# Kernel tuning notes

Hardware: AMD Instinct MI355X
Metric: run time of the kernel (lower is better)

The kernel has to match this reference:

```python
import jax, jax.numpy as jnp
import numpy as np

NL, DM, DI, DS, DR, DC = 4, 1024, 2048, 16, 64, 4
B, L, DLOC, NC = 8, 224, 672, 10
EPS = 1e-5


def _rmsnorm(h, w):
    return h * jax.lax.rsqrt(jnp.mean(h * h, axis=-1, keepdims=True) + EPS) * w


def setup_inputs() -> dict:
    key = jax.random.key(0)
    ks = jax.random.split(key, 10)
    s = 0.02
    return dict(
        x=jax.random.normal(ks[0], (B, L, DLOC), jnp.float32),
        w_proj=jax.random.normal(ks[1], (DLOC, DM), jnp.float32) * s,
        b_proj=jnp.zeros((DM,), jnp.float32),
        norm_w=jnp.ones((NL, DM), jnp.float32),
        w_in=jax.random.normal(ks[2], (NL, DM, 2 * DI), jnp.float32) * s,
        w_conv=jax.random.normal(ks[3], (NL, DI, DC), jnp.float32) * s,
        b_conv=jnp.zeros((NL, DI), jnp.float32),
        w_x=jax.random.normal(ks[4], (NL, DI, DR + 2 * DS), jnp.float32) * s,
        w_dt=jax.random.normal(ks[5], (NL, DR, DI), jnp.float32) * s,
        b_dt=jax.random.normal(ks[6], (NL, DI), jnp.float32) * 0.1,
        A_log=jnp.broadcast_to(jnp.log(jnp.arange(1, DS + 1, dtype=jnp.float32)), (NL, DI, DS)) + jnp.zeros((NL, DI, DS), jnp.float32),
        Dp=jnp.ones((NL, DI), jnp.float32),
        w_out=jax.random.normal(ks[7], (NL, DI, DM), jnp.float32) * s,
        final_norm_w=jnp.ones((DM,), jnp.float32),
        w_fc=jax.random.normal(ks[8], (DM, NC), jnp.float32) * s,
        b_fc=jnp.zeros((NC,), jnp.float32),
    )


def reference(x, w_proj, b_proj, norm_w, w_in, w_conv, b_conv, w_x, w_dt, b_dt, A_log, Dp, w_out, final_norm_w, w_fc, b_fc):
    # input_proj: (B,L,DLOC) -> (B,L,DM)
    h = x @ w_proj + b_proj
    for l in range(NL):
        xn = _rmsnorm(h, norm_w[l])
        xz = xn @ w_in[l]                      # (B,L,2*DI)
        xp, z = jnp.split(xz, 2, axis=-1)
        # causal depthwise conv1d along L, kernel size DC
        xpad = jnp.pad(xp, ((0, 0), (DC - 1, 0), (0, 0)))
        xc = sum(xpad[:, k:k + L, :] * w_conv[l][:, k] for k in range(DC)) + b_conv[l]
        xc = jax.nn.silu(xc)
        x_dbl = xc @ w_x[l]                    # (B,L,DR+2*DS)
        dtr, Bm, Cm = jnp.split(x_dbl, [DR, DR + DS], axis=-1)
        dt = jax.nn.softplus(dtr @ w_dt[l] + b_dt[l])   # (B,L,DI)
        A = -jnp.exp(A_log[l])                 # (DI,DS)
        xs = (jnp.swapaxes(dt, 0, 1), jnp.swapaxes(Bm, 0, 1),
              jnp.swapaxes(Cm, 0, 1), jnp.swapaxes(xc, 0, 1))

        def step(hs, inp):
            dt_t, B_t, C_t, u_t = inp          # (B,DI),(B,DS),(B,DS),(B,DI)
            dA = jnp.exp(dt_t[:, :, None] * A)                        # (B,DI,DS)
            hs = dA * hs + (dt_t * u_t)[:, :, None] * B_t[:, None, :]
            y = jnp.einsum('bds,bs->bd', hs, C_t)
            return hs, y

        h0 = jnp.zeros((B, DI, DS), x.dtype)
        _, ys = jax.lax.scan(step, h0, xs)     # ys: (L,B,DI)
        y = jnp.swapaxes(ys, 0, 1) + Dp[l] * xc
        y = y * jax.nn.silu(z)
        h = h + y @ w_out[l]
    h = _rmsnorm(h, final_norm_w)
    pooled = h[:, -1, :]                       # last-token pooling
    return pooled @ w_fc + b_fc                # (B,NC)
```

## Files before the change

### kernel.cpp

```cpp
#include <hip/hip_runtime.h>
#include <hip/hip_bf16.h>
#include <hip/hip_fp16.h>
#include <math.h>

#define NL 4
#define DM 1024
#define DI 2048
#define DS 16
#define DR 64
#define DC 4
#define B_ 8
#define L_ 224
#define DLOC 672
#define NC 10
#define EPS 1e-5f

#define ROWS (B_ * L_)

typedef unsigned short u16;
typedef __attribute__((ext_vector_type(8))) short bf16x8;
typedef __attribute__((ext_vector_type(4))) float f32x4;
typedef __attribute__((address_space(1))) const void gvoid_t;
typedef __attribute__((address_space(3))) void lvoid_t;

__device__ __forceinline__ u16 f2bf(float f) {
  union { float f; unsigned int u; } v;
  v.f = f;
  unsigned int u = v.u;
  return (u16)((u + 0x7fffu + ((u >> 16) & 1u)) >> 16);
}

__device__ __forceinline__ void load4h(const __half* p, float* o) {
  uint2 r = *(const uint2*)p;
  __half2 h0 = *(__half2*)&r.x;
  __half2 h1 = *(__half2*)&r.y;
  float2 f0 = __half22float2(h0);
  float2 f1 = __half22float2(h1);
  o[0] = f0.x; o[1] = f0.y; o[2] = f1.x; o[3] = f1.y;
}

__device__ __forceinline__ void load8h(const __half* p, float* o) {
  uint4 r = *(const uint4*)p;
  __half2 h0 = *(__half2*)&r.x;
  __half2 h1 = *(__half2*)&r.y;
  __half2 h2 = *(__half2*)&r.z;
  __half2 h3 = *(__half2*)&r.w;
  float2 f0 = __half22float2(h0);
  float2 f1 = __half22float2(h1);
  float2 f2 = __half22float2(h2);
  float2 f3 = __half22float2(h3);
  o[0] = f0.x; o[1] = f0.y; o[2] = f1.x; o[3] = f1.y;
  o[4] = f2.x; o[5] = f2.y; o[6] = f3.x; o[7] = f3.y;
}

template <int ACC, int BROW, int TSTORE, int ACT, int SPLITK, typename OT>
__global__ __launch_bounds__(256) void gemm_bt_mfma(
    const u16* __restrict__ A, const u16* __restrict__ Bt,
    const float* __restrict__ bias, OT* __restrict__ C, int K, int lda,
    int ldb, int ldc) {
  if (SPLITK) {
    A += (size_t)blockIdx.z * SPLITK;
    Bt += (size_t)blockIdx.z * SPLITK;
  }
  __shared__ __align__(16) u16 As[128 * 32];
  __shared__ __align__(16) u16 Bs[128 * 32];
  const int tid = threadIdx.x;
  const int lane = tid & 63;
  const int wv = tid >> 6;
  const int n0 = blockIdx.x * 128;
  const int m0 = blockIdx.y * 128;
  const int wm0 = (wv & 1) * 64;
  const int wn0 = (wv >> 1) * 64;
  const int quad = lane >> 4;
  const int l16 = lane & 15;

  const int srow = wv * 32 + (lane >> 2);
  const int scol = (lane & 3) * 8;
  const u16* ga0 = A + (size_t)(m0 + srow) * lda + scol;
  const u16* ga1 = ga0 + (size_t)16 * lda;
  const u16* gb0 = Bt + (size_t)(n0 + srow) * ldb + scol;
  const u16* gb1 = gb0 + (size_t)16 * ldb;
  u16* la0 = &As[(wv * 32) * 32];
  u16* la1 = &As[(wv * 32 + 16) * 32];
  u16* lb0 = &Bs[(wv * 32) * 32];
  u16* lb1 = &Bs[(wv * 32 + 16) * 32];

  f32x4 acc[4][4] = {};

  for (int k0 = 0; k0 < K; k0 += 32) {
    __syncthreads();
    __builtin_amdgcn_global_load_lds((gvoid_t*)ga0, (lvoid_t*)la0, 16, 0, 0);
    __builtin_amdgcn_global_load_lds((gvoid_t*)ga1, (lvoid_t*)la1, 16, 0, 0);
    __builtin_amdgcn_global_load_lds((gvoid_t*)gb0, (lvoid_t*)lb0, 16, 0, 0);
    __builtin_amdgcn_global_load_lds((gvoid_t*)gb1, (lvoid_t*)lb1, 16, 0, 0);
    __syncthreads();
    bf16x8 af[4], bfr[4];
#pragma unroll
    for (int i = 0; i < 4; i++)
      af[i] = *(const bf16x8*)&As[(wm0 + i * 16 + l16) * 32 + quad * 8];
#pragma unroll
    for (int j = 0; j < 4; j++)
      bfr[j] = *(const bf16x8*)&Bs[(wn0 + j * 16 + l16) * 32 + quad * 8];
#pragma unroll
    for (int i = 0; i < 4; i++)
#pragma unroll
      for (int j = 0; j < 4; j++)
        acc[i][j] = __builtin_amdgcn_mfma_f32_16x16x32_bf16(af[i], bfr[j],
                                                            acc[i][j], 0, 0, 0);
    ga0 += 32; ga1 += 32; gb0 += 32; gb1 += 32;
  }

#pragma unroll
  for (int i = 0; i < 4; i++) {
#pragma unroll
    for (int j = 0; j < 4; j++) {
      const int col = n0 + wn0 + j * 16 + l16;
      const int rowb = m0 + wm0 + i * 16 + quad * 4;
      if (TSTORE) {
        __half* Ch = (__half*)C;
        union { __half2 h[2]; uint2 u; } pk;
        pk.h[0].x = __float2half(acc[i][j][0]);
        pk.h[0].y = __float2half(acc[i][j][1]);
        pk.h[1].x = __float2half(acc[i][j][2]);
        pk.h[1].y = __float2half(acc[i][j][3]);
        *(uint2*)(Ch + (size_t)col * ldc + rowb) = pk.u;
      } else {
        float bv = 0.f;
        if (BROW == 1) bv = bias[col];
#pragma unroll
        for (int r = 0; r < 4; r++) {
          float v = acc[i][j][r] + bv;
          if (BROW == 2) v += bias[rowb + r];
          if (ACT == 1) v = (v > 20.f) ? v : log1pf(expf(v));
          OT* p = C + (size_t)(rowb + r) * ldc + col;
          if (ACC == 2) {
            atomicAdd((float*)p, v);
          } else {
            if (ACC == 1) v += (float)*p;
            *p = (OT)v;
          }
        }
      }
    }
  }
}

__device__ __forceinline__ void transpose_cvt_body(
    const float* __restrict__ src, u16* __restrict__ dst, int K, int N,
    int bx, int by, int tid) {
  __shared__ float t[32][33];
  const int n0 = bx * 32;
  const int k0 = by * 32;
  const int c = tid & 31;
  const int r = tid >> 5;
#pragma unroll
  for (int rr = 0; rr < 4; rr++)
    t[r + rr * 8][c] = src[(size_t)(k0 + r + rr * 8) * N + n0 + c];
  __syncthreads();
#pragma unroll
  for (int rr = 0; rr < 4; rr++)
    dst[(size_t)(n0 + r + rr * 8) * K + k0 + c] = f2bf(t[c][r + rr * 8]);
}

__global__ __launch_bounds__(256) void transpose_cvt_kernel(
    const float* __restrict__ src, u16* __restrict__ dst, int K, int N) {
  transpose_cvt_body(src, dst, K, N, blockIdx.x, blockIdx.y, threadIdx.x);
}

__global__ __launch_bounds__(256) void prep_weights_kernel(
    const float* __restrict__ w_in_l, const float* __restrict__ w_out_l,
    const float* __restrict__ w_x_l, const float* __restrict__ w_dt_l,
    u16* __restrict__ winT, u16* __restrict__ woutT, u16* __restrict__ w_x16,
    u16* __restrict__ w_dt16) {
  int bid = blockIdx.x;
  if (bid < 4096) {
    transpose_cvt_body(w_in_l, winT, DM, 2 * DI, bid & 127, bid >> 7,
                       threadIdx.x);
  } else if (bid < 6144) {
    bid -= 4096;
    transpose_cvt_body(w_out_l, woutT, DI, DM, bid & 31, bid >> 5,
                       threadIdx.x);
  } else if (bid < 6336) {
    bid -= 6144;
    transpose_cvt_body(w_x_l, w_x16, DI, 96, bid % 3, bid / 3, threadIdx.x);
  } else {
    bid -= 6336;
    transpose_cvt_body(w_dt_l, w_dt16, DR, DI, bid & 63, bid >> 6,
                       threadIdx.x);
  }
}

__global__ __launch_bounds__(256) void transpose_u16_kernel(
    const u16* __restrict__ src, u16* __restrict__ dst, int K, int N) {
  __shared__ u16 t[32][33];
  const int n0 = blockIdx.x * 32;
  const int k0 = blockIdx.y * 32;
  const int c = threadIdx.x & 31;
  const int r = threadIdx.x >> 5;
#pragma unroll
  for (int rr = 0; rr < 4; rr++)
    t[r + rr * 8][c] = src[(size_t)(k0 + r + rr * 8) * N + n0 + c];
  __syncthreads();
#pragma unroll
  for (int rr = 0; rr < 4; rr++)
    dst[(size_t)(n0 + r + rr * 8) * K + k0 + c] = t[c][r + rr * 8];
}

__global__ __launch_bounds__(256) void cvt_kernel(const float* __restrict__ src,
                                                  u16* __restrict__ dst) {
  const int i = blockIdx.x * 256 + threadIdx.x;
  const float4 v = ((const float4*)src)[i];
  ushort4 o;
  o.x = f2bf(v.x);
  o.y = f2bf(v.y);
  o.z = f2bf(v.z);
  o.w = f2bf(v.w);
  ((ushort4*)dst)[i] = o;
}

__global__ __launch_bounds__(256) void rmsnorm_kernel(
    const float* __restrict__ h, const float* __restrict__ w,
    u16* __restrict__ out) {
  const int row = blockIdx.x;
  const int tid = threadIdx.x;
  const float4 v = *(const float4*)(h + (size_t)row * DM + tid * 4);
  float ss = v.x * v.x + v.y * v.y + v.z * v.z + v.w * v.w;
#pragma unroll
  for (int off = 32; off > 0; off >>= 1) ss += __shfl_xor(ss, off);
  __shared__ float red[4];
  if ((tid & 63) == 0) red[tid >> 6] = ss;
  __syncthreads();
  float tot = red[0] + red[1] + red[2] + red[3];
  const float inv = rsqrtf(tot / (float)DM + EPS);
  const float4 wv = *(const float4*)(w + tid * 4);
  ushort4 o;
  o.x = f2bf(v.x * inv * wv.x);
  o.y = f2bf(v.y * inv * wv.y);
  o.z = f2bf(v.z * inv * wv.z);
  o.w = f2bf(v.w * inv * wv.w);
  *(ushort4*)(out + (size_t)row * DM + tid * 4) = o;
}

__global__ __launch_bounds__(256) void conv_silu_tile_kernel(
    const __half* __restrict__ xpT, const float* __restrict__ wc,
    const float* __restrict__ bc, __half* __restrict__ uT,
    u16* __restrict__ u16rm) {
  __shared__ u16 tile[32][33];
  const int tid = threadIdx.x;
  const int d0 = blockIdx.x * 32;
  const int r0 = blockIdx.y * 32;
  const int dl = tid >> 3;
  const int rq = (tid & 7) * 4;
  const int d = d0 + dl;
  const int r = r0 + rq;
  const int t = r % L_;
  const __half* row = xpT + (size_t)d * ROWS + r;
  float v[4];
  load4h(row, v);
  float p0 = 0.f, p1 = 0.f, p2 = 0.f;
  if (t > 0) {
    p0 = __half2float(row[-3]);
    p1 = __half2float(row[-2]);
    p2 = __half2float(row[-1]);
  }
  const float w0 = wc[d * 4 + 0], w1 = wc[d * 4 + 1], w2 = wc[d * 4 + 2],
              w3 = wc[d * 4 + 3];
  const float bb = bc[d];
  float o[4];
  float s;
  s = bb + p0 * w0 + p1 * w1 + p2 * w2 + v[0] * w3; o[0] = s / (1.f + expf(-s));
  s = bb + p1 * w0 + p2 * w1 + v[0] * w2 + v[1] * w3; o[1] = s / (1.f + expf(-s));
  s = bb + p2 * w0 + v[0] * w1 + v[1] * w2 + v[2] * w3; o[2] = s / (1.f + expf(-s));
  s = bb + v[0] * w0 + v[1] * w1 + v[2] * w2 + v[3] * w3; o[3] = s / (1.f + expf(-s));
  union { __half2 h[2]; uint2 u; } pk;
  pk.h[0].x = __float2half(o[0]); pk.h[0].y = __float2half(o[1]);
  pk.h[1].x = __float2half(o[2]); pk.h[1].y = __float2half(o[3]);
  *(uint2*)(uT + (size_t)d * ROWS + r) = pk.u;
#pragma unroll
  for (int i = 0; i < 4; i++) tile[rq + i][dl] = f2bf(o[i]);
  __syncthreads();
  const int rl = tid >> 3;
  const int dq = (tid & 7) * 4;
  ushort4 ov;
  ov.x = tile[rl][dq + 0];
  ov.y = tile[rl][dq + 1];
  ov.z = tile[rl][dq + 2];
  ov.w = tile[rl][dq + 3];
  *(ushort4*)(u16rm + (size_t)(r0 + rl) * DI + d0 + dq) = ov;
}

__global__ __launch_bounds__(256) void scan_kernel(
    const __half* __restrict__ dtT, const __half* __restrict__ uT,
    const __half* __restrict__ zT, const float* __restrict__ xdblT,
    const float* __restrict__ A_log, const float* __restrict__ Dp,
    u16* __restrict__ yT) {
  __shared__ __align__(16) __half dtu[4][2][512];
  __shared__ __align__(16) __half zbuf[4][2][512];
  __shared__ __align__(16) float bcb[2][32 * 36];

  const int tid = threadIdx.x;
  const int wv = tid >> 6;
  const int lane = tid & 63;
  const int b = blockIdx.x >> 6;
  const int d0 = ((blockIdx.x & 63) << 5) + wv * 8;
  const int c = lane >> 3;
  const int sg = lane & 7;
  const int d = d0 + c;
  const int s0 = sg * 2;

  const int sl = lane & 31;
  const size_t srcoff =
      (size_t)(d0 + (sl & 7)) * ROWS + (size_t)b * L_ + (sl >> 3) * 8;
  const __half* gdtu = (lane < 32 ? dtT : uT) + srcoff;
  const __half* gz = zT + srcoff;

  const int bs = tid >> 3;
  const int bt4 = (tid & 7) * 4;
  const float* gbc = xdblT + (size_t)(DR + bs) * ROWS + (size_t)b * L_ + bt4;

  const float2 Al = *(const float2*)(A_log + (size_t)d * DS + s0);
  const float A20 = -expf(Al.x) * 1.44269504f;
  const float A21 = -expf(Al.y) * 1.44269504f;
  const float Dpd = Dp[d];
  u16* yp = yT + (size_t)d * ROWS + b * L_;

  float hs0 = 0.f, hs1 = 0.f;

  auto stage_dtuz = [&](int t0, int p) {
    __builtin_amdgcn_global_load_lds((gvoid_t*)(gdtu + t0),
                                     (lvoid_t*)&dtu[wv][p][0], 16, 0, 0);
    __builtin_amdgcn_global_load_lds((gvoid_t*)(gz + t0),
                                     (lvoid_t*)&zbuf[wv][p][0], 16, 0, 0);
  };

  {
    float4 bc0 = *(const float4*)gbc;
    stage_dtuz(0, 0);
    __builtin_amdgcn_s_waitcnt(0x0f70);
    *(float4*)&bcb[0][bs * 36 + bt4] = bc0;
    __syncthreads();
  }

  for (int ch = 0; ch < L_ / 32; ch++) {
    const int p = ch & 1;
    const int t0 = ch * 32;
    float4 bcn;
    const bool more = (ch + 1 < L_ / 32);
    if (more) {
      bcn = *(const float4*)(gbc + t0 + 32);
      stage_dtuz(t0 + 32, p ^ 1);
    }
#pragma unroll
    for (int g = 0; g < 4; g++) {
      float dt8[8], u8[8], z8[8];
      load8h(&dtu[wv][p][g * 64 + c * 8], dt8);
      load8h(&dtu[wv][p][256 + g * 64 + c * 8], u8);
      load8h(&zbuf[wv][p][g * 64 + c * 8], z8);
      float Bv0[8], Bv1[8], Cv0[8], Cv1[8];
      *(float4*)&Bv0[0] = *(const float4*)&bcb[p][s0 * 36 + g * 8];
      *(float4*)&Bv0[4] = *(const float4*)&bcb[p][s0 * 36 + g * 8 + 4];
      *(float4*)&Bv1[0] = *(const float4*)&bcb[p][(s0 + 1) * 36 + g * 8];
      *(float4*)&Bv1[4] = *(const float4*)&bcb[p][(s0 + 1) * 36 + g * 8 + 4];
      *(float4*)&Cv0[0] = *(const float4*)&bcb[p][(16 + s0) * 36 + g * 8];
      *(float4*)&Cv0[4] = *(const float4*)&bcb[p][(16 + s0) * 36 + g * 8 + 4];
      *(float4*)&Cv1[0] = *(const float4*)&bcb[p][(17 + s0) * 36 + g * 8];
      *(float4*)&Cv1[4] = *(const float4*)&bcb[p][(17 + s0) * 36 + g * 8 + 4];
      union { u16 h[8]; uint4 v; } yb;
#pragma unroll
      for (int k = 0; k < 8; k++) {
        const float dtv = dt8[k];
        const float uu = u8[k];
        const float du = dtv * uu;
        hs0 = fmaf(hs0, exp2f(dtv * A20), du * Bv0[k]);
        hs1 = fmaf(hs1, exp2f(dtv * A21), du * Bv1[k]);
        float pr = fmaf(hs1, Cv1[k], hs0 * Cv0[k]);
        pr += __shfl_xor(pr, 1);
        pr += __shfl_xor(pr, 2);
        pr += __shfl_xor(pr, 4);
        if (sg == 0) {
          const float zz = z8[k];
          float yv = pr + Dpd * uu;
          yv *= zz / (1.f + expf(-zz));
          yb.h[k] = f2bf(yv);
        }
      }
      if (sg == 0) *(uint4*)(yp + t0 + g * 8) = yb.v;
    }
    if (more) {
      __builtin_amdgcn_s_waitcnt(0x0f70);
      *(float4*)&bcb[p ^ 1][bs * 36 + bt4] = bcn;
    }
    __syncthreads();
  }
}

__global__ __launch_bounds__(256) void final_kernel(
    const float* __restrict__ h, const float* __restrict__ fnw,
    const float* __restrict__ w_fc, const float* __restrict__ b_fc,
    float* __restrict__ out) {
  const int b = blockIdx.x;
  const int tid = threadIdx.x;
  const size_t row = ((size_t)b * L_ + (L_ - 1)) * DM;
  const float4 v = *(const float4*)(h + row + tid * 4);
  float ss = v.x * v.x + v.y * v.y + v.z * v.z + v.w * v.w;
#pragma unroll
  for (int off = 32; off > 0; off >>= 1) ss += __shfl_xor(ss, off);
  __shared__ float red[4];
  if ((tid & 63) == 0) red[tid >> 6] = ss;
  __syncthreads();
  float tot = red[0] + red[1] + red[2] + red[3];
  const float inv = rsqrtf(tot / (float)DM + EPS);
  const float4 wv = *(const float4*)(fnw + tid * 4);
  float hn[4] = {v.x * inv * wv.x, v.y * inv * wv.y, v.z * inv * wv.z,
                 v.w * inv * wv.w};
  float partial[NC];
#pragma unroll
  for (int j = 0; j < NC; j++) partial[j] = 0.f;
#pragma unroll
  for (int e = 0; e < 4; e++) {
    const int dd = tid * 4 + e;
#pragma unroll
    for (int j = 0; j < NC; j++)
      partial[j] = fmaf(hn[e], w_fc[dd * NC + j], partial[j]);
  }
  __shared__ float red2[256][NC];
  for (int j = 0; j < NC; j++) red2[tid][j] = partial[j];
  __syncthreads();
  for (int stride = 128; stride > 0; stride >>= 1) {
    if (tid < stride)
      for (int j = 0; j < NC; j++) red2[tid][j] += red2[tid + stride][j];
    __syncthreads();
  }
  if (tid < NC) out[b * NC + tid] = red2[0][tid] + b_fc[tid];
}

extern "C" void kernel_launch(void* const* d_in, const int* in_sizes, int n_in,
                              void* d_out, int out_size, void* d_ws,
                              size_t ws_size, hipStream_t stream) {
  const float* x = (const float*)d_in[0];
  const float* w_proj = (const float*)d_in[1];
  const float* b_proj = (const float*)d_in[2];
  const float* norm_w = (const float*)d_in[3];
  const float* w_in = (const float*)d_in[4];
  const float* w_conv = (const float*)d_in[5];
  const float* b_conv = (const float*)d_in[6];
  const float* w_x = (const float*)d_in[7];
  const float* w_dt = (const float*)d_in[8];
  const float* b_dt = (const float*)d_in[9];
  const float* A_log = (const float*)d_in[10];
  const float* Dp = (const float*)d_in[11];
  const float* w_out = (const float*)d_in[12];
  const float* fnw = (const float*)d_in[13];
  const float* w_fc = (const float*)d_in[14];
  const float* b_fc = (const float*)d_in[15];
  float* out = (float*)d_out;

  float* ws = (float*)d_ws;
  float* h = ws;
  float* p1 = h + 1835008;
  __half* xzT = (__half*)p1;
  float* p2 = p1 + 3670016;
  __half* uT = (__half*)p2;
  float* p3 = p2 + 1835008;
  float* xdblT = p3;
  float* p4 = p3 + 229376;
  __half* dtT = (__half*)p4;
  float* p5 = p4 + 1835008;
  u16* yT = (u16*)p5;
  float* p6 = p5 + 1835008;
  u16* y16 = (u16*)p6;
  u16* xn16 = y16;
  float* p7 = p6 + 1835008;
  u16* u16rm = (u16*)p7;
  float* p8 = p7 + 1835008;
  u16* x16 = (u16*)p8;
  float* p9 = p8 + 602112;
  u16* wprojT = (u16*)p9;
  float* p10 = p9 + 344064;
  u16* winT = (u16*)p10;
  float* p11 = p10 + 2097152;
  u16* woutT = (u16*)p11;
  float* p12 = p11 + 1048576;
  u16* w_x16 = (u16*)p12;
  float* p13 = p12 + 131072;
  u16* w_dt16 = (u16*)p13;
  float* p14 = p13 + 65536;
  u16* dtr16 = (u16*)p14;

  const dim3 blk(256);

  cvt_kernel<<<ROWS * DLOC / 1024, blk, 0, stream>>>(x, x16);
  transpose_cvt_kernel<<<dim3(DM / 32, DLOC / 32), blk, 0, stream>>>(
      w_proj, wprojT, DLOC, DM);

  gemm_bt_mfma<0, 1, 0, 0, 0, float>
      <<<dim3(DM / 128, ROWS / 128), blk, 0, stream>>>(
          x16, wprojT, b_proj, h, DLOC, DLOC, DLOC, DM);

  for (int l = 0; l < NL; l++) {
    prep_weights_kernel<<<6464, blk, 0, stream>>>(
        w_in + (size_t)l * DM * 2 * DI, w_out + (size_t)l * DI * DM,
        w_x + (size_t)l * DI * 96, w_dt + (size_t)l * DR * DI, winT, woutT,
        w_x16, w_dt16);

    rmsnorm_kernel<<<ROWS, blk, 0, stream>>>(h, norm_w + (size_t)l * DM, xn16);
    gemm_bt_mfma<0, 0, 1, 0, 0, __half>
        <<<dim3(2 * DI / 128, ROWS / 128), blk, 0, stream>>>(
            xn16, winT, nullptr, (__half*)xzT, DM, DM, DM, ROWS);
    conv_silu_tile_kernel<<<dim3(DI / 32, ROWS / 32), blk, 0, stream>>>(
        xzT, w_conv + (size_t)l * DI * DC, b_conv + (size_t)l * DI, uT, u16rm);
    hipMemsetAsync(xdblT, 0, (size_t)128 * ROWS * sizeof(float), stream);
    gemm_bt_mfma<2, 0, 0, 0, 512, float>
        <<<dim3(ROWS / 128, 1, 4), blk, 0, stream>>>(
            w_x16, u16rm, nullptr, xdblT, 512, DI, DI, ROWS);
    transpose_cvt_kernel<<<dim3(ROWS / 32, DR / 32), blk, 0, stream>>>(
        xdblT, dtr16, DR, ROWS);
    gemm_bt_mfma<0, 2, 0, 1, 0, __half>
        <<<dim3(ROWS / 128, DI / 128), blk, 0, stream>>>(
            w_dt16, dtr16, b_dt + (size_t)l * DI, dtT, DR, DR, DR, ROWS);
    scan_kernel<<<dim3(B_ * (DI / 32)), blk, 0, stream>>>(
        dtT, uT, xzT + (size_t)DI * ROWS, xdblT, A_log + (size_t)l * DI * DS,
        Dp + (size_t)l * DI, yT);
    transpose_u16_kernel<<<dim3(ROWS / 32, DI / 32), blk, 0, stream>>>(
        yT, y16, DI, ROWS);
    gemm_bt_mfma<1, 0, 0, 0, 0, float>
        <<<dim3(DM / 128, ROWS / 128), blk, 0, stream>>>(
            y16, woutT, nullptr, h, DI, DI, DI, DM);
  }

  final_kernel<<<B_, blk, 0, stream>>>(h, fnw, w_fc, b_fc, out);
}
```

Measured before the change: 1.069 ms.

## Replace sequential selective scan with chunked three-pass scan in row-major layout

Replaces the single sequential scan kernel with a chunked parallel scan. A per-chunk state pass computes 16-step partial states and summed dt, a combine pass propagates carries across 14 chunks, and an apply pass recomputes outputs from the carried-in states. Intermediates (z, u, dt, y) move to row-major layout, which removes the y transpose kernel and the transposed dtr conversion, and the in-projection GEMM is split into separate x and z outputs. The goal is far more parallelism across the L dimension and fewer transpose passes, at the cost of extra state traffic and recomputing the recurrence twice.

```diff
diff --git a/kernel.cpp b/kernel.cpp
--- a/kernel.cpp
+++ b/kernel.cpp
@@ -16,6 +16,8 @@
 #define EPS 1e-5f
 
 #define ROWS (B_ * L_)
+#define NCHK 14
+#define CHS 16
 
 typedef unsigned short u16;
 typedef __attribute__((ext_vector_type(8))) short bf16x8;
@@ -37,20 +39,6 @@
   float2 f0 = __half22float2(h0);
   float2 f1 = __half22float2(h1);
   o[0] = f0.x; o[1] = f0.y; o[2] = f1.x; o[3] = f1.y;
-}
-
-__device__ __forceinline__ void load8h(const __half* p, float* o) {
-  uint4 r = *(const uint4*)p;
-  __half2 h0 = *(__half2*)&r.x;
-  __half2 h1 = *(__half2*)&r.y;
-  __half2 h2 = *(__half2*)&r.z;
-  __half2 h3 = *(__half2*)&r.w;
-  float2 f0 = __half22float2(h0);
-  float2 f1 = __half22float2(h1);
-  float2 f2 = __half22float2(h2);
-  float2 f3 = __half22float2(h3);
-  o[0] = f0.x; o[1] = f0.y; o[2] = f1.x; o[3] = f1.y;
-  o[4] = f2.x; o[5] = f2.y; o[6] = f3.x; o[7] = f3.y;
 }
 
 template <int ACC, int BROW, int TSTORE, int ACT, int SPLITK, typename OT>
@@ -190,22 +178,6 @@
   }
 }
 
-__global__ __launch_bounds__(256) void transpose_u16_kernel(
-    const u16* __restrict__ src, u16* __restrict__ dst, int K, int N) {
-  __shared__ u16 t[32][33];
-  const int n0 = blockIdx.x * 32;
-  const int k0 = blockIdx.y * 32;
-  const int c = threadIdx.x & 31;
-  const int r = threadIdx.x >> 5;
-#pragma unroll
-  for (int rr = 0; rr < 4; rr++)
-    t[r + rr * 8][c] = src[(size_t)(k0 + r + rr * 8) * N + n0 + c];
-  __syncthreads();
-#pragma unroll
-  for (int rr = 0; rr < 4; rr++)
-    dst[(size_t)(n0 + r + rr * 8) * K + k0 + c] = t[c][r + rr * 8];
-}
-
 __global__ __launch_bounds__(256) void cvt_kernel(const float* __restrict__ src,
                                                   u16* __restrict__ dst) {
   const int i = blockIdx.x * 256 + threadIdx.x;
@@ -218,6 +190,16 @@
   ((ushort4*)dst)[i] = o;
 }
 
+__global__ __launch_bounds__(256) void cvt_dtr_kernel(
+    const float* __restrict__ x_dbl, u16* __restrict__ dtr) {
+  const int e = (blockIdx.x * 256 + threadIdx.x) * 4;
+  const int r = e >> 6, cc = e & 63;
+  const float4 v = *(const float4*)(x_dbl + (size_t)r * 128 + cc);
+  ushort4 o;
+  o.x = f2bf(v.x); o.y = f2bf(v.y); o.z = f2bf(v.z); o.w = f2bf(v.w);
+  *(ushort4*)(dtr + (size_t)r * 64 + cc) = o;
+}
+
 __global__ __launch_bounds__(256) void rmsnorm_kernel(
     const float* __restrict__ h, const float* __restrict__ w,
     u16* __restrict__ out) {
@@ -243,9 +225,10 @@
 
 __global__ __launch_bounds__(256) void conv_silu_tile_kernel(
     const __half* __restrict__ xpT, const float* __restrict__ wc,
-    const float* __restrict__ bc, __half* __restrict__ uT,
-    u16* __restrict__ u16rm) {
+    const float* __restrict__ bc, u16* __restrict__ u16rm,
+    __half* __restrict__ u_rm) {
   __shared__ u16 tile[32][33];
+  __shared__ u16 tileh[32][33];
   const int tid = threadIdx.x;
   const int d0 = blockIdx.x * 32;
   const int r0 = blockIdx.y * 32;
@@ -272,125 +255,174 @@
   s = bb + p1 * w0 + p2 * w1 + v[0] * w2 + v[1] * w3; o[1] = s / (1.f + expf(-s));
   s = bb + p2 * w0 + v[0] * w1 + v[1] * w2 + v[2] * w3; o[2] = s / (1.f + expf(-s));
   s = bb + v[0] * w0 + v[1] * w1 + v[2] * w2 + v[3] * w3; o[3] = s / (1.f + expf(-s));
-  union { __half2 h[2]; uint2 u; } pk;
-  pk.h[0].x = __float2half(o[0]); pk.h[0].y = __float2half(o[1]);
-  pk.h[1].x = __float2half(o[2]); pk.h[1].y = __float2half(o[3]);
-  *(uint2*)(uT + (size_t)d * ROWS + r) = pk.u;
-#pragma unroll
-  for (int i = 0; i < 4; i++) tile[rq + i][dl] = f2bf(o[i]);
+#pragma unroll
+  for (int i = 0; i < 4; i++) {
+    tile[rq + i][dl] = f2bf(o[i]);
+    tileh[rq + i][dl] = __half_as_ushort(__float2half(o[i]));
+  }
   __syncthreads();
   const int rl = tid >> 3;
   const int dq = (tid & 7) * 4;
-  ushort4 ov;
+  ushort4 ov, oh;
   ov.x = tile[rl][dq + 0];
   ov.y = tile[rl][dq + 1];
   ov.z = tile[rl][dq + 2];
   ov.w = tile[rl][dq + 3];
+  oh.x = tileh[rl][dq + 0];
+  oh.y = tileh[rl][dq + 1];
+  oh.z = tileh[rl][dq + 2];
+  oh.w = tileh[rl][dq + 3];
   *(ushort4*)(u16rm + (size_t)(r0 + rl) * DI + d0 + dq) = ov;
-}
-
-__global__ __launch_bounds__(256) void scan_kernel(
-    const __half* __restrict__ dtT, const __half* __restrict__ uT,
-    const __half* __restrict__ zT, const float* __restrict__ xdblT,
+  *(ushort4*)((u16*)u_rm + (size_t)(r0 + rl) * DI + d0 + dq) = oh;
+}
+
+__global__ __launch_bounds__(64) void scan_state_kernel(
+    const __half* __restrict__ dt_rm, const __half* __restrict__ u_rm,
+    const float* __restrict__ x_dbl, const float* __restrict__ A_log,
+    float* __restrict__ S, float* __restrict__ sumdt) {
+  __shared__ u16 dts[CHS][64];
+  __shared__ u16 us[CHS][64];
+  __shared__ float Bs[CHS][16];
+  const int lane = threadIdx.x;
+  const int c = blockIdx.x, g = blockIdx.y, b = blockIdx.z;
+  const int d = (g << 6) + lane;
+  const size_t rbase = (size_t)b * L_ + c * CHS;
+  {
+    const int tr = lane >> 3, c8 = (lane & 7) << 3;
+    const size_t ro = (rbase + tr) * DI + (g << 6) + c8;
+    *(uint4*)&dts[tr][c8] = *(const uint4*)(dt_rm + ro);
+    *(uint4*)&dts[tr + 8][c8] = *(const uint4*)(dt_rm + ro + (size_t)8 * DI);
+    *(uint4*)&us[tr][c8] = *(const uint4*)(u_rm + ro);
+    *(uint4*)&us[tr + 8][c8] = *(const uint4*)(u_rm + ro + (size_t)8 * DI);
+    const int tb = lane >> 2, q4 = (lane & 3) << 2;
+    *(float4*)&Bs[tb][q4] =
+        *(const float4*)(x_dbl + (rbase + tb) * 128 + 64 + q4);
+  }
+  float A2[DS];
+  const float* al = A_log + (size_t)d * DS;
+#pragma unroll
+  for (int s = 0; s < DS; s++) A2[s] = -expf(al[s]) * 1.44269504f;
+  __syncthreads();
+
+  float hs[DS];
+#pragma unroll
+  for (int s = 0; s < DS; s++) hs[s] = 0.f;
+  float cd = 0.f;
+#pragma unroll 4
+  for (int t = 0; t < CHS; t++) {
+    const float dtv = __half2float(((const __half*)dts)[t * 64 + lane]);
+    const float uu = __half2float(((const __half*)us)[t * 64 + lane]);
+    const float du = dtv * uu;
+    cd += dtv;
+    const float4 B0 = *(const float4*)&Bs[t][0];
+    const float4 B1 = *(const float4*)&Bs[t][4];
+    const float4 B2 = *(const float4*)&Bs[t][8];
+    const float4 B3 = *(const float4*)&Bs[t][12];
+    auto upd = [&](int s0, float4 Bq) {
+      hs[s0 + 0] = fmaf(hs[s0 + 0], exp2f(dtv * A2[s0 + 0]), du * Bq.x);
+      hs[s0 + 1] = fmaf(hs[s0 + 1], exp2f(dtv * A2[s0 + 1]), du * Bq.y);
+      hs[s0 + 2] = fmaf(hs[s0 + 2], exp2f(dtv * A2[s0 + 2]), du * Bq.z);
+      hs[s0 + 3] = fmaf(hs[s0 + 3], exp2f(dtv * A2[s0 + 3]), du * Bq.w);
+    };
+    upd(0, B0); upd(4, B1); upd(8, B2); upd(12, B3);
+  }
+  float* Sp = S + (((size_t)c * B_ + b) * DI + d) * DS;
+#pragma unroll
+  for (int s = 0; s < DS; s++) Sp[s] = hs[s];
+  sumdt[((size_t)c * B_ + b) * DI + d] = cd;
+}
+
+__global__ __launch_bounds__(256) void scan_combine_kernel(
+    float* __restrict__ S, const float* __restrict__ sumdt,
+    const float* __restrict__ A_log) {
+  const int idx = blockIdx.x * 256 + threadIdx.x;
+  const int s = idx & 15;
+  const int d = (idx >> 4) & (DI - 1);
+  const int b = idx >> 15;
+  const float A2 = -expf(A_log[(size_t)d * DS + s]) * 1.44269504f;
+  float hv = 0.f;
+#pragma unroll
+  for (int c = 0; c < NCHK; c++) {
+    const size_t base = ((size_t)c * B_ + b) * DI + d;
+    const size_t ix = base * DS + s;
+    const float Sc = S[ix];
+    const float Dc = exp2f(A2 * sumdt[base]);
+    S[ix] = hv;
+    hv = fmaf(Dc, hv, Sc);
+  }
+}
+
+__global__ __launch_bounds__(64) void scan_apply_kernel(
+    const __half* __restrict__ dt_rm, const __half* __restrict__ u_rm,
+    const __half* __restrict__ z_rm, const float* __restrict__ x_dbl,
     const float* __restrict__ A_log, const float* __restrict__ Dp,
-    u16* __restrict__ yT) {
-  __shared__ __align__(16) __half dtu[4][2][512];
-  __shared__ __align__(16) __half zbuf[4][2][512];
-  __shared__ __align__(16) float bcb[2][32 * 36];
-
-  const int tid = threadIdx.x;
-  const int wv = tid >> 6;
-  const int lane = tid & 63;
-  const int b = blockIdx.x >> 6;
-  const int d0 = ((blockIdx.x & 63) << 5) + wv * 8;
-  const int c = lane >> 3;
-  const int sg = lane & 7;
-  const int d = d0 + c;
-  const int s0 = sg * 2;
-
-  const int sl = lane & 31;
-  const size_t srcoff =
-      (size_t)(d0 + (sl & 7)) * ROWS + (size_t)b * L_ + (sl >> 3) * 8;
-  const __half* gdtu = (lane < 32 ? dtT : uT) + srcoff;
-  const __half* gz = zT + srcoff;
-
-  const int bs = tid >> 3;
-  const int bt4 = (tid & 7) * 4;
-  const float* gbc = xdblT + (size_t)(DR + bs) * ROWS + (size_t)b * L_ + bt4;
-
-  const float2 Al = *(const float2*)(A_log + (size_t)d * DS + s0);
-  const float A20 = -expf(Al.x) * 1.44269504f;
-  const float A21 = -expf(Al.y) * 1.44269504f;
+    const float* __restrict__ HS, u16* __restrict__ y_rm) {
+  __shared__ u16 dts[CHS][64];
+  __shared__ u16 us[CHS][64];
+  __shared__ u16 zs[CHS][64];
+  __shared__ float Bs[CHS][16];
+  __shared__ float Cs[CHS][16];
+  const int lane = threadIdx.x;
+  const int c = blockIdx.x, g = blockIdx.y, b = blockIdx.z;
+  const int d = (g << 6) + lane;
+  const size_t rbase = (size_t)b * L_ + c * CHS;
+  {
+    const int tr = lane >> 3, c8 = (lane & 7) << 3;
+    const size_t ro = (rbase + tr) * DI + (g << 6) + c8;
+    *(uint4*)&dts[tr][c8] = *(const uint4*)(dt_rm + ro);
+    *(uint4*)&dts[tr + 8][c8] = *(const uint4*)(dt_rm + ro + (size_t)8 * DI);
+    *(uint4*)&us[tr][c8] = *(const uint4*)(u_rm + ro);
+    *(uint4*)&us[tr + 8][c8] = *(const uint4*)(u_rm + ro + (size_t)8 * DI);
+    *(uint4*)&zs[tr][c8] = *(const uint4*)(z_rm + ro);
+    *(uint4*)&zs[tr + 8][c8] = *(const uint4*)(z_rm + ro + (size_t)8 * DI);
+    const int tb = lane >> 2, q4 = (lane & 3) << 2;
+    *(float4*)&Bs[tb][q4] =
+        *(const float4*)(x_dbl + (rbase + tb) * 128 + 64 + q4);
+    *(float4*)&Cs[tb][q4] =
+        *(const float4*)(x_dbl + (rbase + tb) * 128 + 80 + q4);
+  }
+  float A2[DS];
+  const float* al = A_log + (size_t)d * DS;
+#pragma unroll
+  for (int s = 0; s < DS; s++) A2[s] = -expf(al[s]) * 1.44269504f;
+  float hs[DS];
+  const float* hp = HS + (((size_t)c * B_ + b) * DI + d) * DS;
+#pragma unroll
+  for (int s = 0; s < DS; s++) hs[s] = hp[s];
   const float Dpd = Dp[d];
-  u16* yp = yT + (size_t)d * ROWS + b * L_;
-
-  float hs0 = 0.f, hs1 = 0.f;
-
-  auto stage_dtuz = [&](int t0, int p) {
-    __builtin_amdgcn_global_load_lds((gvoid_t*)(gdtu + t0),
-                                     (lvoid_t*)&dtu[wv][p][0], 16, 0, 0);
-    __builtin_amdgcn_global_load_lds((gvoid_t*)(gz + t0),
-                                     (lvoid_t*)&zbuf[wv][p][0], 16, 0, 0);
-  };
-
-  {
-    float4 bc0 = *(const float4*)gbc;
-    stage_dtuz(0, 0);
-    __builtin_amdgcn_s_waitcnt(0x0f70);
-    *(float4*)&bcb[0][bs * 36 + bt4] = bc0;
-    __syncthreads();
-  }
-
-  for (int ch = 0; ch < L_ / 32; ch++) {
-    const int p = ch & 1;
-    const int t0 = ch * 32;
-    float4 bcn;
-    const bool more = (ch + 1 < L_ / 32);
-    if (more) {
-      bcn = *(const float4*)(gbc + t0 + 32);
-      stage_dtuz(t0 + 32, p ^ 1);
-    }
-#pragma unroll
-    for (int g = 0; g < 4; g++) {
-      float dt8[8], u8[8], z8[8];
-      load8h(&dtu[wv][p][g * 64 + c * 8], dt8);
-      load8h(&dtu[wv][p][256 + g * 64 + c * 8], u8);
-      load8h(&zbuf[wv][p][g * 64 + c * 8], z8);
-      float Bv0[8], Bv1[8], Cv0[8], Cv1[8];
-      *(float4*)&Bv0[0] = *(const float4*)&bcb[p][s0 * 36 + g * 8];
-      *(float4*)&Bv0[4] = *(const float4*)&bcb[p][s0 * 36 + g * 8 + 4];
-      *(float4*)&Bv1[0] = *(const float4*)&bcb[p][(s0 + 1) * 36 + g * 8];
-      *(float4*)&Bv1[4] = *(const float4*)&bcb[p][(s0 + 1) * 36 + g * 8 + 4];
-      *(float4*)&Cv0[0] = *(const float4*)&bcb[p][(16 + s0) * 36 + g * 8];
-      *(float4*)&Cv0[4] = *(const float4*)&bcb[p][(16 + s0) * 36 + g * 8 + 4];
-      *(float4*)&Cv1[0] = *(const float4*)&bcb[p][(17 + s0) * 36 + g * 8];
-      *(float4*)&Cv1[4] = *(const float4*)&bcb[p][(17 + s0) * 36 + g * 8 + 4];
-      union { u16 h[8]; uint4 v; } yb;
-#pragma unroll
-      for (int k = 0; k < 8; k++) {
-        const float dtv = dt8[k];
-        const float uu = u8[k];
-        const float du = dtv * uu;
-        hs0 = fmaf(hs0, exp2f(dtv * A20), du * Bv0[k]);
-        hs1 = fmaf(hs1, exp2f(dtv * A21), du * Bv1[k]);
-        float pr = fmaf(hs1, Cv1[k], hs0 * Cv0[k]);
-        pr += __shfl_xor(pr, 1);
-        pr += __shfl_xor(pr, 2);
-        pr += __shfl_xor(pr, 4);
-        if (sg == 0) {
-          const float zz = z8[k];
-          float yv = pr + Dpd * uu;
-          yv *= zz / (1.f + expf(-zz));
-          yb.h[k] = f2bf(yv);
-        }
-      }
-      if (sg == 0) *(uint4*)(yp + t0 + g * 8) = yb.v;
-    }
-    if (more) {
-      __builtin_amdgcn_s_waitcnt(0x0f70);
-      *(float4*)&bcb[p ^ 1][bs * 36 + bt4] = bcn;
-    }
-    __syncthreads();
+  u16* yp = y_rm + rbase * DI + d;
+  __syncthreads();
+
+#pragma unroll 4
+  for (int t = 0; t < CHS; t++) {
+    const float dtv = __half2float(((const __half*)dts)[t * 64 + lane]);
+    const float uu = __half2float(((const __half*)us)[t * 64 + lane]);
+    const float zz = __half2float(((const __half*)zs)[t * 64 + lane]);
+    const float du = dtv * uu;
+    const float4 B0 = *(const float4*)&Bs[t][0];
+    const float4 B1 = *(const float4*)&Bs[t][4];
+    const float4 B2 = *(const float4*)&Bs[t][8];
+    const float4 B3 = *(const float4*)&Bs[t][12];
+    const float4 C0 = *(const float4*)&Cs[t][0];
+    const float4 C1 = *(const float4*)&Cs[t][4];
+    const float4 C2 = *(const float4*)&Cs[t][8];
+    const float4 C3 = *(const float4*)&Cs[t][12];
+    float p0 = 0.f, p1 = 0.f, p2 = 0.f, p3 = 0.f;
+    auto upd = [&](int s0, float4 Bq, float4 Cq) {
+      hs[s0 + 0] = fmaf(hs[s0 + 0], exp2f(dtv * A2[s0 + 0]), du * Bq.x);
+      p0 = fmaf(hs[s0 + 0], Cq.x, p0);
+      hs[s0 + 1] = fmaf(hs[s0 + 1], exp2f(dtv * A2[s0 + 1]), du * Bq.y);
+      p1 = fmaf(hs[s0 + 1], Cq.y, p1);
+      hs[s0 + 2] = fmaf(hs[s0 + 2], exp2f(dtv * A2[s0 + 2]), du * Bq.z);
+      p2 = fmaf(hs[s0 + 2], Cq.z, p2);
+      hs[s0 + 3] = fmaf(hs[s0 + 3], exp2f(dtv * A2[s0 + 3]), du * Bq.w);
+      p3 = fmaf(hs[s0 + 3], Cq.w, p3);
+    };
+    upd(0, B0, C0); upd(4, B1, C1); upd(8, B2, C2); upd(12, B3, C3);
+    float y = fmaf(Dpd, uu, (p0 + p1) + (p2 + p3));
+    const float e = exp2f(-zz * 1.44269504f);
+    y *= zz * __builtin_amdgcn_rcpf(1.f + e);
+    yp[(size_t)t * DI] = f2bf(y);
   }
 }
 
@@ -457,47 +489,39 @@
 
   float* ws = (float*)d_ws;
   float* h = ws;
-  float* p1 = h + 1835008;
-  __half* xzT = (__half*)p1;
-  float* p2 = p1 + 3670016;
-  __half* uT = (__half*)p2;
-  float* p3 = p2 + 1835008;
-  float* xdblT = p3;
-  float* p4 = p3 + 229376;
-  __half* dtT = (__half*)p4;
-  float* p5 = p4 + 1835008;
-  u16* yT = (u16*)p5;
-  float* p6 = p5 + 1835008;
-  u16* y16 = (u16*)p6;
-  u16* xn16 = y16;
-  float* p7 = p6 + 1835008;
-  u16* u16rm = (u16*)p7;
-  float* p8 = p7 + 1835008;
-  u16* x16 = (u16*)p8;
-  float* p9 = p8 + 602112;
-  u16* wprojT = (u16*)p9;
-  float* p10 = p9 + 344064;
-  u16* winT = (u16*)p10;
-  float* p11 = p10 + 2097152;
-  u16* woutT = (u16*)p11;
-  float* p12 = p11 + 1048576;
-  u16* w_x16 = (u16*)p12;
-  float* p13 = p12 + 131072;
-  u16* w_dt16 = (u16*)p13;
-  float* p14 = p13 + 65536;
-  u16* dtr16 = (u16*)p14;
+  float* p = h + 1835008;
+  __half* xpT = (__half*)p;    p += 1835008;
+  __half* z_rm = (__half*)p;   p += 1835008;
+  __half* u_rm = (__half*)p;   p += 1835008;
+  __half* dt_rm = (__half*)p;  p += 1835008;
+  u16* u16rm = (u16*)p;        p += 1835008;
+  u16* y_rm = (u16*)p;         p += 1835008;
+  u16* xn16 = y_rm;
+  float* x_dbl = p;            p += 229376;
+  float* Sbuf = p;             p += 3670016;
+  float* sumdt = p;            p += 229376;
+  u16* x16 = (u16*)p;          p += 602112;
+  u16* wprojT = (u16*)p;       p += 344064;
+  u16* winT = (u16*)p;         p += 2097152;
+  u16* woutT = (u16*)p;        p += 1048576;
+  u16* w_x16 = (u16*)p;        p += 131072;
+  u16* w_dt16 = (u16*)p;       p += 65536;
+  u16* dtr16 = (u16*)p;        p += 57344;
 
   const dim3 blk(256);
 
   cvt_kernel<<<ROWS * DLOC / 1024, blk, 0, stream>>>(x, x16);
   transpose_cvt_kernel<<<dim3(DM / 32, DLOC / 32), blk, 0, stream>>>(
       w_proj, wprojT, DLOC, DM);
+  hipMemsetAsync(w_x16 + (size_t)96 * DI, 0, (size_t)32 * DI * sizeof(u16),
+                 stream);
 
   gemm_bt_mfma<0, 1, 0, 0, 0, float>
       <<<dim3(DM / 128, ROWS / 128), blk, 0, stream>>>(
           x16, wprojT, b_proj, h, DLOC, DLOC, DLOC, DM);
 
   for (int l = 0; l < NL; l++) {
+    const float* Al = A_log + (size_t)l * DI * DS;
     prep_weights_kernel<<<6464, blk, 0, stream>>>(
         w_in + (size_t)l * DM * 2 * DI, w_out + (size_t)l * DI * DM,
         w_x + (size_t)l * DI * 96, w_dt + (size_t)l * DR * DI, winT, woutT,
@@ -505,27 +529,31 @@
 
     rmsnorm_kernel<<<ROWS, blk, 0, stream>>>(h, norm_w + (size_t)l * DM, xn16);
     gemm_bt_mfma<0, 0, 1, 0, 0, __half>
-        <<<dim3(2 * DI / 128, ROWS / 128), blk, 0, stream>>>(
-            xn16, winT, nullptr, (__half*)xzT, DM, DM, DM, ROWS);
+        <<<dim3(DI / 128, ROWS / 128), blk, 0, stream>>>(
+            xn16, winT, nullptr, xpT, DM, DM, DM, ROWS);
+    gemm_bt_mfma<0, 0, 0, 0, 0, __half>
+        <<<dim3(DI / 128, ROWS / 128), blk, 0, stream>>>(
+            xn16, winT + (size_t)2048 * DM, nullptr, z_rm, DM, DM, DM, DI);
     conv_silu_tile_kernel<<<dim3(DI / 32, ROWS / 32), blk, 0, stream>>>(
-        xzT, w_conv + (size_t)l * DI * DC, b_conv + (size_t)l * DI, uT, u16rm);
-    hipMemsetAsync(xdblT, 0, (size_t)128 * ROWS * sizeof(float), stream);
+        xpT, w_conv + (size_t)l * DI * DC, b_conv + (size_t)l * DI, u16rm,
+        u_rm);
+    hipMemsetAsync(x_dbl, 0, (size_t)ROWS * 128 * sizeof(float), stream);
     gemm_bt_mfma<2, 0, 0, 0, 512, float>
-        <<<dim3(ROWS / 128, 1, 4), blk, 0, stream>>>(
-            w_x16, u16rm, nullptr, xdblT, 512, DI, DI, ROWS);
-    transpose_cvt_kernel<<<dim3(ROWS / 32, DR / 32), blk, 0, stream>>>(
-        xdblT, dtr16, DR, ROWS);
-    gemm_bt_mfma<0, 2, 0, 1, 0, __half>
-        <<<dim3(ROWS / 128, DI / 128), blk, 0, stream>>>(
-            w_dt16, dtr16, b_dt + (size_t)l * DI, dtT, DR, DR, DR, ROWS);
-    scan_kernel<<<dim3(B_ * (DI / 32)), blk, 0, stream>>>(
-        dtT, uT, xzT + (size_t)DI * ROWS, xdblT, A_log + (size_t)l * DI * DS,
-        Dp + (size_t)l * DI, yT);
-    transpose_u16_kernel<<<dim3(ROWS / 32, DI / 32), blk, 0, stream>>>(
-        yT, y16, DI, ROWS);
+        <<<dim3(1, ROWS / 128, 4), blk, 0, stream>>>(
+            u16rm, w_x16, nullptr, x_dbl, 512, DI, DI, 128);
+    cvt_dtr_kernel<<<ROWS * 64 / 1024, blk, 0, stream>>>(x_dbl, dtr16);
+    gemm_bt_mfma<0, 1, 0, 1, 0, __half>
+        <<<dim3(DI / 128, ROWS / 128), blk, 0, stream>>>(
+            dtr16, w_dt16, b_dt + (size_t)l * DI, dt_rm, DR, DR, DR, DI);
+    scan_state_kernel<<<dim3(NCHK, DI / 64, B_), dim3(64), 0, stream>>>(
+        dt_rm, u_rm, x_dbl, Al, Sbuf, sumdt);
+    scan_combine_kernel<<<B_ * DI * DS / 256, blk, 0, stream>>>(Sbuf, sumdt,
+                                                                Al);
+    scan_apply_kernel<<<dim3(NCHK, DI / 64, B_), dim3(64), 0, stream>>>(
+        dt_rm, u_rm, z_rm, x_dbl, Al, Dp + (size_t)l * DI, Sbuf, y_rm);
     gemm_bt_mfma<1, 0, 0, 0, 0, float>
         <<<dim3(DM / 128, ROWS / 128), blk, 0, stream>>>(
-            y16, woutT, nullptr, h, DI, DI, DI, DM);
+            y_rm, woutT, nullptr, h, DI, DI, DI, DM);
   }
 
   final_kernel<<<B_, blk, 0, stream>>>(h, fnw, w_fc, b_fc, out);
```

Result: slower. 1.430 ms (+33.7%).
